# Optimization experiments

Hardware: AMD Instinct MI355X
Metric: run time of the kernel (lower is better)

The kernel has to match this reference:

```python
import jax, jax.numpy as jnp
import numpy as np

ALPHA = 0.2  # LeakyReLU negative slope


def setup_inputs() -> dict:
    key = jax.random.key(0)
    k1, k2, k3, k4 = jax.random.split(key, 4)
    n, t, N, c, o = 16, 12, 64, 64, 64
    inp = jax.random.normal(k1, (n, t, N, c), dtype=jnp.float32)
    adj = jax.random.uniform(k2, (t, N, N), dtype=jnp.float32)
    # xavier_uniform with gain=1.414 ~ U(-b, b), b = gain*sqrt(6/(fan_in+fan_out))
    bW = 1.414 * np.sqrt(6.0 / (c + o))
    W = jax.random.uniform(k3, (c, o), dtype=jnp.float32, minval=-bW, maxval=bW)
    ba = 1.414 * np.sqrt(6.0 / (2 * o + 1))
    a = jax.random.uniform(k4, (2 * o, 1), dtype=jnp.float32, minval=-ba, maxval=ba)
    return {"inp": inp, "adj": adj, "W": W, "a": a}


def reference(inp, adj, W, a):
    n, t, N, c = inp.shape
    o = W.shape[1]
    # h: [n,t,N,o]
    h = jnp.einsum('ntvc,co->ntvo', inp, W)
    # Literal translation of the torch repeat/cat(dim=1)/view sequence
    a1 = jnp.tile(h, (1, 1, 1, N)).reshape(n, t, N * N, o)   # row v*N+w -> h[v]
    a2 = jnp.tile(h, (1, 1, N, 1))                            # row v*N+w -> h[w]
    # NOTE: original concatenates along dim=1 (time axis), then row-major views
    # to [n,t,N,N,2o]; we reproduce that exact reshape semantics.
    a_input = jnp.concatenate([a1, a2], axis=1).reshape(n, t, N, N, 2 * o)
    e = jax.nn.leaky_relu(
        jnp.einsum('ntvwo,of->ntvwf', a_input, a), negative_slope=ALPHA
    )[..., 0]                                                  # [n,t,N,N]
    # adj path is dead code in the original: both branches set attention = e
    attention = jax.nn.softmax(e, axis=3)
    # dropout with training=False -> identity
    h_prime = jnp.einsum('ntvw,ntwh->ntvh', attention, h)     # [n,t,N,o]
    return jax.nn.elu(h_prime), attention
```

## Files before the change

kernel.cpp:

```cpp
#include <hip/hip_runtime.h>

#define ALPHA 0.2f

__device__ __forceinline__ float leaky(float x){ return x > 0.f ? x : ALPHA * x; }
__device__ __forceinline__ float elu1 (float x){ return x > 0.f ? x : (__expf(x) - 1.f); }

__global__ __launch_bounds__(512) void gat_fused(
    const float* __restrict__ inp,
    const float* __restrict__ W,
    const float* __restrict__ av,
    float* __restrict__ out)
{
    __shared__ __align__(16) float Ws[64*68];
    __shared__ __align__(16) float X [64*68];
    __shared__ __align__(16) float H [64*68];
    __shared__ __align__(16) float aL[128];
    __shared__ __align__(16) float WaA[64], WaB[64], Wa1[64];
    __shared__ float sArr[2][64];
    __shared__ float S0L[64], S1L[64];
    __shared__ __align__(16) float attL[2][32];
    __shared__ __align__(16) float eluL[2][64];

    const int bid = blockIdx.x;
    const int nI  = bid / 12;
    const int tP  = bid - nI * 12;
    const int tid = threadIdx.x;

    const bool firstHalf = (tP < 6);
    const int tt0 = firstHalf ? 2*tP : 2*tP - 12;
    const int tt1 = tt0 + 1;

    const size_t ownBase = (size_t)(nI*12 + tP) * 4096;

    float4 rr[16];
    if (tid < 128) {
        const int q  = tid >> 6, vvl = tid & 63;
        const int ttq = q ? tt1 : tt0;
        const float4* xr = (const float4*)(inp + (size_t)(nI*12 + ttq)*4096 + vvl*64);
        #pragma unroll
        for (int u = 0; u < 16; ++u) rr[u] = xr[u];
    }

    const float4* W4 = (const float4*)W;
    const float4* X4 = (const float4*)(inp + ownBase);
    #pragma unroll
    for (int i = tid; i < 1024; i += 512) {
        const int r = i >> 4, c4 = (i & 15) << 2;
        *(float4*)&Ws[r*68 + c4] = W4[i];
        *(float4*)&X [r*68 + c4] = X4[i];
    }
    if (tid < 128) aL[tid] = av[tid];
    __syncthreads();

    if (tid < 64) {
        const float4* wr4 = (const float4*)&Ws[tid*68];
        const float4* a4  = (const float4*)aL;
        float sA = 0.f, sB = 0.f;
        #pragma unroll
        for (int u = 0; u < 16; ++u) {
            const float4 w = wr4[u], x = a4[u], y = a4[u+16];
            sA += w.x*x.x + w.y*x.y + w.z*x.z + w.w*x.w;
            sB += w.x*y.x + w.y*y.y + w.z*y.z + w.w*y.w;
        }
        WaA[tid] = sA; WaB[tid] = sB; Wa1[tid] = sA + sB;
    }

    {
        const int v = tid >> 3, tk = tid & 7;
        float a0=0,a1=0,a2=0,a3=0,a4=0,a5=0,a6=0,a7=0;
        const float* xr = &X[v*68];
        #pragma unroll
        for (int c = 0; c < 64; ++c) {
            const float xv = xr[c];
            const float4* wr4 = (const float4*)&Ws[c*68 + tk*8];
            const float4 w0 = wr4[0], w1 = wr4[1];
            a0 += xv*w0.x; a1 += xv*w0.y; a2 += xv*w0.z; a3 += xv*w0.w;
            a4 += xv*w1.x; a5 += xv*w1.y; a6 += xv*w1.z; a7 += xv*w1.w;
        }
        float* hr = &H[v*68 + tk*8];
        *(float4*)hr       = make_float4(a0,a1,a2,a3);
        *(float4*)(hr + 4) = make_float4(a4,a5,a6,a7);
    }
    __syncthreads();

    if (tid < 128) {
        const int q = tid >> 6, vvl = tid & 63;
        const float* wv = firstHalf ? Wa1 : ((vvl & 1) ? WaB : WaA);
        const float4* wv4 = (const float4*)wv;
        float s = 0.f;
        #pragma unroll
        for (int u = 0; u < 16; ++u) {
            const float4 x = rr[u], w = wv4[u];
            s += x.x*w.x + x.y*w.y + x.z*w.z + x.w*w.w;
        }
        sArr[q][vvl] = s;
    } else if (firstHalf) {
        if (tid < 192) {
            const int k = tid - 128;
            float s0 = 0.f, s1 = 0.f;
            #pragma unroll
            for (int w = 0; w < 32; ++w) { s0 += H[w*68 + k]; s1 += H[(w+32)*68 + k]; }
            S0L[k] = s0; S1L[k] = s1;
        }
    } else {
        if (tid < 384) {
            const int idx = tid - 128;
            const int wp = idx >> 5, k0 = (idx & 31) << 1;
        }
        if (tid < 384) {
            const int idx = tid - 128;
            const int wp = idx >> 3, k0 = (idx & 7) * 8;
            const float4* h0 = (const float4*)&H[wp*68 + k0];
            const float4* h1 = (const float4*)&H[(wp+32)*68 + k0];
            float4 u0 = h0[0], u1 = h0[1], v0 = h1[0], v1 = h1[1];
            float4 r0 = make_float4(u0.x+v0.x, u0.y+v0.y, u0.z+v0.z, u0.w+v0.w);
            float4 r1 = make_float4(u1.x+v1.x, u1.y+v1.y, u1.z+v1.z, u1.w+v1.w);
            *(float4*)&X[wp*68 + k0]     = r0;
            *(float4*)&X[wp*68 + k0 + 4] = r1;
        }
    }
    __syncthreads();

    float* out1 = out + ownBase;
    float* out2 = out + 786432 + ownBase;

    if (firstHalf) {
        const int v = tid >> 3, tk = tid & 7;
        const int q = v >> 5, vp = v & 31;
        const float A = leaky(sArr[q][2*vp]);
        const float B = leaky(sArr[q][2*vp + 1]);
        const float m  = fmaxf(A, B);
        const float eA = __expf(A - m), eB = __expf(B - m);
        const float inv = 1.f / (32.f * (eA + eB));
        const float pA = eA * inv, pB = eB * inv;
        const int k0 = tk * 8;
        float4 r0, r1;
        r0.x = elu1(pA*S0L[k0+0] + pB*S1L[k0+0]);
        r0.y = elu1(pA*S0L[k0+1] + pB*S1L[k0+1]);
        r0.z = elu1(pA*S0L[k0+2] + pB*S1L[k0+2]);
        r0.w = elu1(pA*S0L[k0+3] + pB*S1L[k0+3]);
        r1.x = elu1(pA*S0L[k0+4] + pB*S1L[k0+4]);
        r1.y = elu1(pA*S0L[k0+5] + pB*S1L[k0+5]);
        r1.z = elu1(pA*S0L[k0+6] + pB*S1L[k0+6]);
        r1.w = elu1(pA*S0L[k0+7] + pB*S1L[k0+7]);
        float4* o1 = (float4*)(out1 + v*64 + k0);
        o1[0] = r0; o1[1] = r1;
        const float pv = (tk < 4) ? pA : pB;
        const float4 p4 = make_float4(pv, pv, pv, pv);
        float4* o2 = (float4*)(out2 + v*64 + k0);
        o2[0] = p4; o2[1] = p4;
    } else {
        if (tid < 64) {
            const int q = tid >> 5, wp = tid & 31;
            float cv = leaky(sArr[q][2*wp] + sArr[q][2*wp + 1]);
            float m = cv;
            #pragma unroll
            for (int mask = 16; mask; mask >>= 1) m = fmaxf(m, __shfl_xor(m, mask));
            const float e = __expf(cv - m);
            float s = e;
            #pragma unroll
            for (int mask = 16; mask; mask >>= 1) s += __shfl_xor(s, mask);
            attL[q][wp] = e / (2.f * s);
        }
        __syncthreads();
        if (tid < 128) {
            const int q = tid >> 6, k = tid & 63;
            float acc = 0.f;
            #pragma unroll
            for (int wp = 0; wp < 32; ++wp)
                acc += attL[q][wp] * X[wp*68 + k];
            eluL[q][k] = elu1(acc);
        }
        __syncthreads();
        const int v = tid >> 3, tk = tid & 7;
        const int q = v >> 5;
        const int k0 = tk * 8;
        const float4* s1 = (const float4*)&eluL[q][k0];
        float4* o1 = (float4*)(out1 + v*64 + k0);
        o1[0] = s1[0]; o1[1] = s1[1];
        const float4* s2 = (const float4*)&attL[q][(tk & 3)*8];
        float4* o2 = (float4*)(out2 + v*64 + k0);
        o2[0] = s2[0]; o2[1] = s2[1];
    }
}

extern "C" void kernel_launch(void* const* d_in, const int* in_sizes, int n_in,
                              void* d_out, int out_size, void* d_ws, size_t ws_size,
                              hipStream_t stream) {
    const float* inp = (const float*)d_in[0];
    const float* W   = (const float*)d_in[2];
    const float* av  = (const float*)d_in[3];
    float* out = (float*)d_out;
    gat_fused<<<dim3(192), dim3(512), 0, stream>>>(inp, W, av, out);
}
```

Before: 66.82 us.

## Hold W column in registers and restructure the projection GEMM

Each thread now keeps one column of W (64 floats) in registers, loaded straight from global memory. It computes 8 rows of H with broadcast float4 reads of X, replacing the earlier shared-memory W tile loop. This cuts LDS traffic in the projection, and the sArr dot product now shares a phase with the GEMM, removing one barrier. The column-sum and pair-sum reductions move into the later branch phases, which adds an extra barrier inside each branch. The 64 extra registers per thread at 512 threads raise register pressure and may cause spills.

New measurement: 68.44 us. 1.02x slower.

```diff
diff --git a/kernel.cpp b/kernel.cpp
--- a/kernel.cpp
+++ b/kernel.cpp
@@ -17,7 +17,7 @@
     __shared__ __align__(16) float aL[128];
     __shared__ __align__(16) float WaA[64], WaB[64], Wa1[64];
     __shared__ float sArr[2][64];
-    __shared__ float S0L[64], S1L[64];
+    __shared__ __align__(16) float S0L[64], S1L[64];
     __shared__ __align__(16) float attL[2][32];
     __shared__ __align__(16) float eluL[2][64];
 
@@ -25,18 +25,22 @@
     const int nI  = bid / 12;
     const int tP  = bid - nI * 12;
     const int tid = threadIdx.x;
+    const int lane = tid & 63;
+    const int wvid = tid >> 6;
 
     const bool firstHalf = (tP < 6);
     const int tt0 = firstHalf ? 2*tP : 2*tP - 12;
-    const int tt1 = tt0 + 1;
 
     const size_t ownBase = (size_t)(nI*12 + tP) * 4096;
+
+    float wreg[64];
+    #pragma unroll
+    for (int c = 0; c < 64; ++c) wreg[c] = W[c*64 + lane];
 
     float4 rr[16];
     if (tid < 128) {
         const int q  = tid >> 6, vvl = tid & 63;
-        const int ttq = q ? tt1 : tt0;
-        const float4* xr = (const float4*)(inp + (size_t)(nI*12 + ttq)*4096 + vvl*64);
+        const float4* xr = (const float4*)(inp + (size_t)(nI*12 + tt0 + q)*4096 + vvl*64);
         #pragma unroll
         for (int u = 0; u < 16; ++u) rr[u] = xr[u];
     }
@@ -64,29 +68,12 @@
         }
         WaA[tid] = sA; WaB[tid] = sB; Wa1[tid] = sA + sB;
     }
-
-    {
-        const int v = tid >> 3, tk = tid & 7;
-        float a0=0,a1=0,a2=0,a3=0,a4=0,a5=0,a6=0,a7=0;
-        const float* xr = &X[v*68];
-        #pragma unroll
-        for (int c = 0; c < 64; ++c) {
-            const float xv = xr[c];
-            const float4* wr4 = (const float4*)&Ws[c*68 + tk*8];
-            const float4 w0 = wr4[0], w1 = wr4[1];
-            a0 += xv*w0.x; a1 += xv*w0.y; a2 += xv*w0.z; a3 += xv*w0.w;
-            a4 += xv*w1.x; a5 += xv*w1.y; a6 += xv*w1.z; a7 += xv*w1.w;
-        }
-        float* hr = &H[v*68 + tk*8];
-        *(float4*)hr       = make_float4(a0,a1,a2,a3);
-        *(float4*)(hr + 4) = make_float4(a4,a5,a6,a7);
-    }
     __syncthreads();
 
     if (tid < 128) {
         const int q = tid >> 6, vvl = tid & 63;
-        const float* wv = firstHalf ? Wa1 : ((vvl & 1) ? WaB : WaA);
-        const float4* wv4 = (const float4*)wv;
+        const float* wvp = firstHalf ? Wa1 : ((vvl & 1) ? WaB : WaA);
+        const float4* wv4 = (const float4*)wvp;
         float s = 0.f;
         #pragma unroll
         for (int u = 0; u < 16; ++u) {
@@ -94,30 +81,23 @@
             s += x.x*w.x + x.y*w.y + x.z*w.z + x.w*w.w;
         }
         sArr[q][vvl] = s;
-    } else if (firstHalf) {
-        if (tid < 192) {
-            const int k = tid - 128;
-            float s0 = 0.f, s1 = 0.f;
+    }
+
+    {
+        const int vbase = wvid * 8;
+        float acc[8];
+        #pragma unroll
+        for (int r = 0; r < 8; ++r) acc[r] = 0.f;
+        #pragma unroll
+        for (int c0 = 0; c0 < 64; c0 += 4) {
             #pragma unroll
-            for (int w = 0; w < 32; ++w) { s0 += H[w*68 + k]; s1 += H[(w+32)*68 + k]; }
-            S0L[k] = s0; S1L[k] = s1;
+            for (int r = 0; r < 8; ++r) {
+                const float4 xb = *(const float4*)&X[(vbase + r)*68 + c0];
+                acc[r] += xb.x*wreg[c0] + xb.y*wreg[c0+1] + xb.z*wreg[c0+2] + xb.w*wreg[c0+3];
+            }
         }
-    } else {
-        if (tid < 384) {
-            const int idx = tid - 128;
-            const int wp = idx >> 5, k0 = (idx & 31) << 1;
-        }
-        if (tid < 384) {
-            const int idx = tid - 128;
-            const int wp = idx >> 3, k0 = (idx & 7) * 8;
-            const float4* h0 = (const float4*)&H[wp*68 + k0];
-            const float4* h1 = (const float4*)&H[(wp+32)*68 + k0];
-            float4 u0 = h0[0], u1 = h0[1], v0 = h1[0], v1 = h1[1];
-            float4 r0 = make_float4(u0.x+v0.x, u0.y+v0.y, u0.z+v0.z, u0.w+v0.w);
-            float4 r1 = make_float4(u1.x+v1.x, u1.y+v1.y, u1.z+v1.z, u1.w+v1.w);
-            *(float4*)&X[wp*68 + k0]     = r0;
-            *(float4*)&X[wp*68 + k0 + 4] = r1;
-        }
+        #pragma unroll
+        for (int r = 0; r < 8; ++r) H[(vbase + r)*68 + lane] = acc[r];
     }
     __syncthreads();
 
@@ -125,6 +105,14 @@
     float* out2 = out + 786432 + ownBase;
 
     if (firstHalf) {
+        if (tid < 64) {
+            const int k = tid;
+            float s0 = 0.f, s1 = 0.f;
+            #pragma unroll
+            for (int w = 0; w < 32; ++w) { s0 += H[w*68 + k]; s1 += H[(w+32)*68 + k]; }
+            S0L[k] = s0; S1L[k] = s1;
+        }
+        __syncthreads();
         const int v = tid >> 3, tk = tid & 7;
         const int q = v >> 5, vp = v & 31;
         const float A = leaky(sArr[q][2*vp]);
@@ -134,15 +122,17 @@
         const float inv = 1.f / (32.f * (eA + eB));
         const float pA = eA * inv, pB = eB * inv;
         const int k0 = tk * 8;
+        const float4 s00 = *(const float4*)&S0L[k0],     s01 = *(const float4*)&S0L[k0+4];
+        const float4 s10 = *(const float4*)&S1L[k0],     s11 = *(const float4*)&S1L[k0+4];
         float4 r0, r1;
-        r0.x = elu1(pA*S0L[k0+0] + pB*S1L[k0+0]);
-        r0.y = elu1(pA*S0L[k0+1] + pB*S1L[k0+1]);
-        r0.z = elu1(pA*S0L[k0+2] + pB*S1L[k0+2]);
-        r0.w = elu1(pA*S0L[k0+3] + pB*S1L[k0+3]);
-        r1.x = elu1(pA*S0L[k0+4] + pB*S1L[k0+4]);
-        r1.y = elu1(pA*S0L[k0+5] + pB*S1L[k0+5]);
-        r1.z = elu1(pA*S0L[k0+6] + pB*S1L[k0+6]);
-        r1.w = elu1(pA*S0L[k0+7] + pB*S1L[k0+7]);
+        r0.x = elu1(pA*s00.x + pB*s10.x);
+        r0.y = elu1(pA*s00.y + pB*s10.y);
+        r0.z = elu1(pA*s00.z + pB*s10.z);
+        r0.w = elu1(pA*s00.w + pB*s10.w);
+        r1.x = elu1(pA*s01.x + pB*s11.x);
+        r1.y = elu1(pA*s01.y + pB*s11.y);
+        r1.z = elu1(pA*s01.z + pB*s11.z);
+        r1.w = elu1(pA*s01.w + pB*s11.w);
         float4* o1 = (float4*)(out1 + v*64 + k0);
         o1[0] = r0; o1[1] = r1;
         const float pv = (tk < 4) ? pA : pB;
@@ -161,6 +151,14 @@
             #pragma unroll
             for (int mask = 16; mask; mask >>= 1) s += __shfl_xor(s, mask);
             attL[q][wp] = e / (2.f * s);
+        } else if (tid >= 128 && tid < 384) {
+            const int idx = tid - 128;
+            const int wp = idx >> 3, k0 = (idx & 7) * 8;
+            const float4* h0 = (const float4*)&H[wp*68 + k0];
+            const float4* h1 = (const float4*)&H[(wp+32)*68 + k0];
+            const float4 u0 = h0[0], u1 = h0[1], v0 = h1[0], v1 = h1[1];
+            *(float4*)&X[wp*68 + k0]     = make_float4(u0.x+v0.x, u0.y+v0.y, u0.z+v0.z, u0.w+v0.w);
+            *(float4*)&X[wp*68 + k0 + 4] = make_float4(u1.x+v1.x, u1.y+v1.y, u1.z+v1.z, u1.w+v1.w);
         }
         __syncthreads();
         if (tid < 128) {
```
